# Optimization experiments

Hardware: AMD Instinct MI355X
Metric: run time of the kernel (lower is better)

## Reference

```python
import jax, jax.numpy as jnp
import numpy as np

B, L, DM = 4, 409, 192            # batch, tokens (1 cls + 16 target + 196 template + 196 search), d_model
DI, DS, DR, K, DEPTH = 384, 16, 12, 4, 24   # d_inner=2*DM, d_state, dt_rank=ceil(DM/16), d_conv, depth
EPS = 1e-5


def setup_inputs() -> dict:
    key = jax.random.key(0)
    ks = list(jax.random.split(key, 16))
    def rn(i, shape, s=0.02):
        return jax.random.normal(ks[i], shape, jnp.float32) * s
    # S4D-real init: A = [1..d_state] per channel, stored as log
    A_log = jnp.log(jnp.tile(jnp.arange(1, DS + 1, dtype=jnp.float32), (DEPTH, DI, 1)))
    return {
        "tokens": jax.random.normal(ks[0], (B, L, DM), jnp.float32),
        "norm_w": jnp.ones((DEPTH, DM), jnp.float32),
        "in_proj_w": rn(1, (DEPTH, 2 * DI, DM)),
        "conv_w": rn(2, (DEPTH, DI, 1, K), 0.2),
        "conv_b": jnp.zeros((DEPTH, DI), jnp.float32),
        "conv_w_b": rn(3, (DEPTH, DI, 1, K), 0.2),
        "conv_b_b": jnp.zeros((DEPTH, DI), jnp.float32),
        "x_proj_w": rn(4, (DEPTH, DR + 2 * DS, DI)),
        "x_proj_w_b": rn(5, (DEPTH, DR + 2 * DS, DI)),
        "dt_proj_w": rn(6, (DEPTH, DI, DR), 0.1),
        "dt_bias": rn(7, (DEPTH, DI), 0.5),
        "dt_proj_w_b": rn(8, (DEPTH, DI, DR), 0.1),
        "dt_bias_b": rn(9, (DEPTH, DI), 0.5),
        "A_log": A_log,
        "A_log_b": A_log,
        "D_param": jnp.ones((DEPTH, DI), jnp.float32),
        "D_param_b": jnp.ones((DEPTH, DI), jnp.float32),
        "out_proj_w": rn(10, (DEPTH, DM, DI)),
        "norm_f_w": jnp.ones((DM,), jnp.float32),
    }


def _rms(x, w):
    return x * jax.lax.rsqrt(jnp.mean(x * x, -1, keepdims=True) + EPS) * w


def _causal_conv(x, w, b):
    # x [B,L,DI]; depthwise causal conv1d, kernel K (pad left K-1)
    y = jax.lax.conv_general_dilated(
        jnp.swapaxes(x, 1, 2), w, (1,), [(K - 1, 0)],
        dimension_numbers=("NCH", "OIH", "NCH"), feature_group_count=DI)
    return jnp.swapaxes(y + b[None, :, None], 1, 2)


def _selective_scan(u, delta, A, Bm, Cm, Dp):
    # u,delta [B,L,DI]; A [DI,DS]; Bm,Cm [B,L,DS]; Dp [DI]
    def step(h, inp):
        u_t, d_t, b_t, c_t = inp  # [B,DI],[B,DI],[B,DS],[B,DS]
        h = h * jnp.exp(d_t[..., None] * A) + (d_t * u_t)[..., None] * b_t[:, None, :]
        return h, jnp.einsum("bdn,bn->bd", h, c_t)
    h0 = jnp.zeros((u.shape[0], A.shape[0], A.shape[1]), u.dtype)
    xs = tuple(jnp.swapaxes(t, 0, 1) for t in (u, delta, Bm, Cm))
    _, ys = jax.lax.scan(step, h0, xs)
    return jnp.swapaxes(ys, 0, 1) + u * Dp


def _scan_dir(xin, cw, cb, xpw, dtw, dtb, a_log, dp):
    xf = jax.nn.silu(_causal_conv(xin, cw, cb))
    x_dbl = jnp.einsum("bld,ed->ble", xf, xpw)
    dt, Bm, Cm = jnp.split(x_dbl, [DR, DR + DS], axis=-1)
    dt = jax.nn.softplus(jnp.einsum("blr,dr->bld", dt, dtw) + dtb)
    return _selective_scan(xf, dt, -jnp.exp(a_log), Bm, Cm, dp)


def _mixer(x, p):
    # bimamba v2: forward scan + backward (flipped) scan with separate params
    xz = jnp.einsum("bld,ed->ble", x, p["in_proj_w"])
    xin, z = jnp.split(xz, 2, axis=-1)
    y_f = _scan_dir(xin, p["conv_w"], p["conv_b"], p["x_proj_w"],
                    p["dt_proj_w"], p["dt_bias"], p["A_log"], p["D_param"])
    y_b = _scan_dir(xin[:, ::-1], p["conv_w_b"], p["conv_b_b"], p["x_proj_w_b"],
                    p["dt_proj_w_b"], p["dt_bias_b"], p["A_log_b"], p["D_param_b"])[:, ::-1]
    y = (y_f + y_b) * jax.nn.silu(z) * 0.5   # z-gating + if_divide_out
    return jnp.einsum("ble,de->bld", y, p["out_proj_w"])


def reference(tokens, norm_w, in_proj_w, conv_w, conv_b, conv_w_b, conv_b_b,
              x_proj_w, x_proj_w_b, dt_proj_w, dt_bias, dt_proj_w_b, dt_bias_b,
              A_log, A_log_b, D_param, D_param_b, out_proj_w, norm_f_w):
    stacked = {"norm_w": norm_w, "in_proj_w": in_proj_w,
               "conv_w": conv_w, "conv_b": conv_b, "conv_w_b": conv_w_b, "conv_b_b": conv_b_b,
               "x_proj_w": x_proj_w, "x_proj_w_b": x_proj_w_b,
               "dt_proj_w": dt_proj_w, "dt_bias": dt_bias,
               "dt_proj_w_b": dt_proj_w_b, "dt_bias_b": dt_bias_b,
               "A_log": A_log, "A_log_b": A_log_b,
               "D_param": D_param, "D_param_b": D_param_b,
               "out_proj_w": out_proj_w}

    def layer(carry, p):
        hidden, residual = carry
        residual = residual + hidden          # add (first layer: residual starts at 0)
        h = _rms(residual, p["norm_w"])       # fused_add_norm prenorm path (RMSNorm)
        h = _mixer(h, p)
        return (h, residual), None

    init = (tokens, jnp.zeros_like(tokens))
    (hidden, residual), _ = jax.lax.scan(layer, init, stacked)
    return _rms(residual + hidden, norm_f_w)
```

## Files before the change

### kernel.cpp

```cpp
#include <hip/hip_runtime.h>
#include <hip/hip_cooperative_groups.h>
#include <math.h>

namespace cg = cooperative_groups;

#define BB     4
#define LLEN   409
#define DMODEL 192
#define DINNER 384
#define DSTATE 16
#define DRANK  12
#define KCONV  4
#define NLAYER 24
#define NROW   (BB*LLEN)
#define EPSF   1e-5f
#define CH2    16
#define NCH2   26

#define OFF_A    12288
#define OFF_RS   16128
#define OFF_DTIN 16144
#define SMEMF    16336

#define NT_NORMIN  1236
#define NT_CONV    (2*NROW*96)
#define NT_XP2     206
#define NT_SCANP   312
#define NT_GATEOUT 309

__device__ __forceinline__ float siluf(float x){ return x/(1.f+__expf(-x)); }
__device__ __forceinline__ float softplusf(float x){ return (x>20.f)? x : log1pf(__expf(x)); }

struct MP {
  const float *norm_w, *conv_w, *conv_b, *conv_w_b, *conv_b_b;
  const float *dt_bias, *dt_bias_b, *D_param, *D_param_b, *norm_f_w;
  float *residual, *xz, *xf_f, *xf_b, *dtbc_f, *dtbc_b, *dt_f, *dt_b, *y_f, *y_b;
  float *q_buf, *sdt_buf;
  float *WtIn, *WtXpPF, *WtXpPB, *WtDtF, *WtDtB, *WtOut, *AnTF, *AnTB;
  float *out;
};

__global__ void k_init(const float* __restrict__ t, float* __restrict__ r, int n){
  int i = blockIdx.x*256+threadIdx.x;
  if (i<n) r[i]=t[i];
}

__global__ __launch_bounds__(256) void k_txp(const float* __restrict__ src,
    float* __restrict__ dst, int R, int C, int RP){
  __shared__ float t[32][33];
  int l = blockIdx.z;
  int c0 = blockIdx.x*32, r0 = blockIdx.y*32;
  const float* s = src + (size_t)l*R*C;
  float* d = dst + (size_t)l*C*RP;
  int tx = threadIdx.x, ty = threadIdx.y;
  #pragma unroll
  for (int yy=ty; yy<32; yy+=8){
    int rr = r0+yy, cc = c0+tx;
    t[yy][tx] = (rr<R && cc<C)? s[(size_t)rr*C+cc] : 0.f;
  }
  __syncthreads();
  #pragma unroll
  for (int yy=ty; yy<32; yy+=8){
    int cc = c0+yy, rr = r0+tx;
    if (cc<C && rr<RP) d[(size_t)cc*RP+rr] = t[tx][yy];
  }
}

__global__ void k_negexpT2(const float* __restrict__ a, float* __restrict__ o, int n){
  int i = blockIdx.x*256+threadIdx.x;
  if (i<n){
    int l = i/(DINNER*DSTATE); int rem = i%(DINNER*DSTATE);
    int nn = rem/DINNER, d = rem%DINNER;
    o[i] = -expf(a[((size_t)l*DINNER + d)*DSTATE + nn]);
  }
}

__device__ void ph_normin(float* sm, int task, int l, const MP& P){
  float* w_lds = sm;
  float* a_lds = sm + OFF_A;
  float* rs_s  = sm + OFF_RS;
  const float* norm_w = P.norm_w + (size_t)l*DMODEL;
  const float* Wt     = P.WtIn   + (size_t)l*DMODEL*768;
  int tid = threadIdx.x;
  int r0 = (task/12)*16, c0 = (task%12)*64;
  #pragma unroll
  for (int s=0;s<12;s++){
    int idx = tid + s*256; int i = idx/DMODEL, k = idx%DMODEL; int row = r0+i;
    a_lds[k*20+i] = (row<NROW)? P.residual[(size_t)row*DMODEL+k] : 0.f;
  }
  {
    int j4 = (tid&15)*4, kr = tid>>4;
    #pragma unroll
    for (int s=0;s<12;s++){
      int k = kr + s*16;
      *reinterpret_cast<float4*>(&w_lds[k*64+j4]) =
        *reinterpret_cast<const float4*>(&Wt[(size_t)k*768 + c0 + j4]);
    }
  }
  __syncthreads();
  int wv = tid>>6, lane = tid&63;
  {
    float ss[4] = {0.f,0.f,0.f,0.f};
    #pragma unroll
    for (int q=0;q<3;q++){
      int k = lane + q*64;
      #pragma unroll
      for (int r=0;r<4;r++){ float v = a_lds[k*20 + wv*4 + r]; ss[r] += v*v; }
    }
    #pragma unroll
    for (int r=0;r<4;r++){
      float s = ss[r];
      #pragma unroll
      for (int off=1; off<64; off<<=1) s += __shfl_xor(s, off, 64);
      if (lane==0) rs_s[wv*4+r] = rsqrtf(s/(float)DMODEL + EPSF);
    }
  }
  __syncthreads();
  #pragma unroll
  for (int s=0;s<12;s++){
    int idx = tid + s*256; int k = idx>>4, i = idx&15;
    a_lds[k*20+i] *= rs_s[i]*norm_w[k];
  }
  __syncthreads();
  int j = tid & 63, rg = tid >> 6;
  float acc[4] = {0.f,0.f,0.f,0.f};
  #pragma unroll 8
  for (int k=0;k<192;k++){
    float w = w_lds[k*64+j];
    float4 a = *reinterpret_cast<const float4*>(&a_lds[k*20 + rg*4]);
    acc[0]+=a.x*w; acc[1]+=a.y*w; acc[2]+=a.z*w; acc[3]+=a.w*w;
  }
  #pragma unroll
  for (int q=0;q<4;q++){
    int row = r0 + rg*4 + q;
    if (row<NROW) P.xz[(size_t)row*768 + c0 + j] = acc[q];
  }
  __syncthreads();
}

__device__ void ph_conv(int i, int l, const MP& P){
  int dir = i / (NROW*96);
  int rem = i - dir*(NROW*96);
  int d4 = (rem % 96)*4; int bl = rem / 96;
  int b = bl / LLEN; int ll = bl % LLEN;
  const float* cw = (dir? P.conv_w_b : P.conv_w) + (size_t)l*DINNER*KCONV;
  const float* cb = (dir? P.conv_b_b : P.conv_b) + (size_t)l*DINNER;
  float4 w0 = *reinterpret_cast<const float4*>(&cw[(d4+0)*KCONV]);
  float4 w1 = *reinterpret_cast<const float4*>(&cw[(d4+1)*KCONV]);
  float4 w2 = *reinterpret_cast<const float4*>(&cw[(d4+2)*KCONV]);
  float4 w3 = *reinterpret_cast<const float4*>(&cw[(d4+3)*KCONV]);
  float4 acc = *reinterpret_cast<const float4*>(&cb[d4]);
  const float* wa0 = (const float*)&w0; const float* wa1 = (const float*)&w1;
  const float* wa2 = (const float*)&w2; const float* wa3 = (const float*)&w3;
  #pragma unroll
  for (int k=0;k<KCONV;k++){
    int o = dir? (LLEN-1-ll-k+3) : (ll-3+k);
    bool ok = dir? (ll+k>=3) : (o>=0);
    if (ok){
      float4 x = *reinterpret_cast<const float4*>(&P.xz[((size_t)(b*LLEN+o))*768 + d4]);
      acc.x += wa0[k]*x.x; acc.y += wa1[k]*x.y; acc.z += wa2[k]*x.z; acc.w += wa3[k]*x.w;
    }
  }
  float* out = dir? P.xf_b : P.xf_f;
  float4 r; r.x = siluf(acc.x); r.y = siluf(acc.y); r.z = siluf(acc.z); r.w = siluf(acc.w);
  *reinterpret_cast<float4*>(&out[(size_t)bl*DINNER + d4]) = r;
}

__device__ void ph_xp2(float* sm, int task, int l, const MP& P){
  float* w_lds  = sm;
  float* a_lds  = sm + OFF_A;
  float* dtin_s = sm + OFF_DTIN;
  int dir = task & 1, rt = task >> 1;
  const float* xf  = dir? P.xf_b : P.xf_f;
  const float* Wxp = (dir? P.WtXpPB : P.WtXpPF) + (size_t)l*DINNER*64;
  const float* Wdt = (dir? P.WtDtB  : P.WtDtF ) + (size_t)l*DRANK*DINNER;
  const float* dtb = (dir? P.dt_bias_b : P.dt_bias) + (size_t)l*DINNER;
  float* dtbc = dir? P.dtbc_b : P.dtbc_f;
  float* dtp  = dir? P.dt_b   : P.dt_f;
  int tid = threadIdx.x, r0 = rt*16;
  int j = tid & 63, rg = tid >> 6;
  float acc[4] = {0.f,0.f,0.f,0.f};
  for (int c=0;c<2;c++){
    int K0 = c*192;
    if (c) __syncthreads();
    {
      int j4 = (tid&15)*4, kr = tid>>4;
      #pragma unroll
      for (int s=0;s<12;s++){
        int k = kr + s*16;
        *reinterpret_cast<float4*>(&w_lds[k*64+j4]) =
          *reinterpret_cast<const float4*>(&Wxp[(size_t)(K0+k)*64 + j4]);
      }
    }
    {
      int i = tid>>4, kc = (tid&15)*12;
      int row = r0+i;
      #pragma unroll
      for (int m=0;m<12;m+=4){
        float4 v = make_float4(0.f,0.f,0.f,0.f);
        if (row<NROW) v = *reinterpret_cast<const float4*>(&xf[(size_t)row*DINNER + K0 + kc + m]);
        a_lds[(kc+m+0)*20+i]=v.x; a_lds[(kc+m+1)*20+i]=v.y;
        a_lds[(kc+m+2)*20+i]=v.z; a_lds[(kc+m+3)*20+i]=v.w;
      }
    }
    __syncthreads();
    #pragma unroll 8
    for (int k=0;k<192;k++){
      float w = w_lds[k*64+j];
      float4 a = *reinterpret_cast<const float4*>(&a_lds[k*20 + rg*4]);
      acc[0]+=a.x*w; acc[1]+=a.y*w; acc[2]+=a.z*w; acc[3]+=a.w*w;
    }
  }
  __syncthreads();
  #pragma unroll
  for (int q=0;q<4;q++){
    int i = rg*4+q, row = r0+i;
    if (j<44 && row<NROW) dtbc[(size_t)row*44 + j] = acc[q];
    if (j<12) dtin_s[i*12 + j] = acc[q];
  }
  __syncthreads();
  for (int idx=tid; idx<12*DINNER; idx+=256) w_lds[idx] = Wdt[idx];
  __syncthreads();
  for (int idx=tid; idx<16*DINNER; idx+=256){
    int i = idx/DINNER, dd = idx - i*DINNER;
    int row = r0+i;
    float v = dtb[dd];
    #pragma unroll
    for (int r=0;r<12;r++) v += dtin_s[i*12+r]*w_lds[r*DINNER+dd];
    if (row<NROW) dtp[(size_t)row*DINNER+dd] = softplusf(v);
  }
  __syncthreads();
}

__device__ void ph_scan1(float* sm, int pair, int l, const MP& P){
  int tid = threadIdx.x;
  int sub = tid>>7, ltid = tid&127;
  int gt  = pair*2 + sub;
  int dir = gt / 312; int rem = gt % 312;
  int bch = rem / 3;  int d0b = rem % 3;
  int b = bch / NCH2, ch = bch % NCH2;
  const float* xf   = dir? P.xf_b  : P.xf_f;
  const float* dtbc = dir? P.dtbc_b: P.dtbc_f;
  const float* dtp  = dir? P.dt_b  : P.dt_f;
  const float* an   = (dir? P.AnTB : P.AnTF) + (size_t)l*DINNER*DSTATE;
  int t0 = ch*CH2;
  int T  = (t0+CH2<=LLEN)? CH2 : (LLEN-t0);
  int d0 = d0b*128;
  size_t base = (size_t)b*LLEN + t0;
  float* dt_s = sm + sub*5120;
  float* u_s  = dt_s + 2048;
  float* B_s  = dt_s + 4096;
  for (int t=0;t<T;t++){
    dt_s[t*128+ltid] = dtp[(base+t)*DINNER + d0 + ltid];
    u_s [t*128+ltid] = xf [(base+t)*DINNER + d0 + ltid];
  }
  for (int idx = ltid; idx < T*16; idx += 128){
    int t = idx>>4, n = idx&15;
    B_s[idx] = dtbc[(base+t)*44 + 12 + n];
  }
  __syncthreads();
  int d = d0 + ltid;
  float A[16], h[16];
  #pragma unroll
  for (int n=0;n<16;n++){ A[n] = an[n*DINNER + d]; h[n] = 0.f; }
  float sdt = 0.f;
  for (int t=0;t<T;t++){
    float dtv = dt_s[t*128+ltid];
    float du  = dtv * u_s[t*128+ltid];
    float Bv[16];
    #pragma unroll
    for (int q=0;q<4;q++) *reinterpret_cast<float4*>(&Bv[q*4]) =
        *reinterpret_cast<const float4*>(&B_s[t*16 + q*4]);
    #pragma unroll
    for (int n=0;n<16;n++) h[n] = h[n]*__expf(dtv*A[n]) + du*Bv[n];
    sdt += dtv;
  }
  size_t ci = ((size_t)dir*BB + b)*NCH2 + ch;
  float* qo = &P.q_buf[(ci*DINNER + d)*DSTATE];
  #pragma unroll
  for (int q=0;q<4;q++) *reinterpret_cast<float4*>(&qo[q*4]) =
      make_float4(h[q*4+0], h[q*4+1], h[q*4+2], h[q*4+3]);
  P.sdt_buf[ci*DINNER + d] = sdt;
  __syncthreads();
}

__device__ void ph_scan2(float* sm, int pair, int l, const MP& P){
  int tid = threadIdx.x;
  int sub = tid>>7, ltid = tid&127;
  int gt  = pair*2 + sub;
  int dir = gt / 312; int rem = gt % 312;
  int bch = rem / 3;  int d0b = rem % 3;
  int b = bch / NCH2, ch = bch % NCH2;
  const float* xf   = dir? P.xf_b  : P.xf_f;
  const float* dtbc = dir? P.dtbc_b: P.dtbc_f;
  const float* dtp  = dir? P.dt_b  : P.dt_f;
  const float* an   = (dir? P.AnTB : P.AnTF) + (size_t)l*DINNER*DSTATE;
  const float* Dp   = (dir? P.D_param_b : P.D_param) + (size_t)l*DINNER;
  float* y = dir? P.y_b : P.y_f;
  int t0 = ch*CH2;
  int T  = (t0+CH2<=LLEN)? CH2 : (LLEN-t0);
  int d0 = d0b*128;
  size_t base = (size_t)b*LLEN + t0;
  float* dt_s = sm + sub*5120;
  float* u_s  = dt_s + 2048;
  float* B_s  = dt_s + 4096;
  float* C_s  = dt_s + 4352;
  for (int t=0;t<T;t++){
    dt_s[t*128+ltid] = dtp[(base+t)*DINNER + d0 + ltid];
    u_s [t*128+ltid] = xf [(base+t)*DINNER + d0 + ltid];
  }
  for (int idx = ltid; idx < T*16; idx += 128){
    int t = idx>>4, n = idx&15;
    B_s[idx] = dtbc[(base+t)*44 + 12 + n];
    C_s[idx] = dtbc[(base+t)*44 + 28 + n];
  }
  __syncthreads();
  int d = d0 + ltid;
  float A[16], h[16];
  #pragma unroll
  for (int n=0;n<16;n++){ A[n] = an[n*DINNER + d]; h[n] = 0.f; }
  size_t sbase = ((size_t)dir*BB + b)*NCH2;
  for (int cc=0; cc<ch; cc++){
    float sv = P.sdt_buf[(sbase+cc)*DINNER + d];
    const float* qp = &P.q_buf[((sbase+cc)*DINNER + d)*DSTATE];
    #pragma unroll
    for (int n=0;n<16;n++) h[n] = qp[n] + __expf(A[n]*sv)*h[n];
  }
  float Dd = Dp[d];
  for (int t=0;t<T;t++){
    float dtv = dt_s[t*128+ltid];
    float u   = u_s [t*128+ltid];
    float du  = dtv*u;
    float Bv[16], Cv[16];
    #pragma unroll
    for (int q=0;q<4;q++){
      *reinterpret_cast<float4*>(&Bv[q*4]) = *reinterpret_cast<const float4*>(&B_s[t*16+q*4]);
      *reinterpret_cast<float4*>(&Cv[q*4]) = *reinterpret_cast<const float4*>(&C_s[t*16+q*4]);
    }
    float y0=0.f, y1=0.f, y2=0.f, y3=0.f;
    #pragma unroll
    for (int n=0;n<16;n+=4){
      h[n+0] = h[n+0]*__expf(dtv*A[n+0]) + du*Bv[n+0];
      h[n+1] = h[n+1]*__expf(dtv*A[n+1]) + du*Bv[n+1];
      h[n+2] = h[n+2]*__expf(dtv*A[n+2]) + du*Bv[n+2];
      h[n+3] = h[n+3]*__expf(dtv*A[n+3]) + du*Bv[n+3];
      y0 += h[n+0]*Cv[n+0]; y1 += h[n+1]*Cv[n+1];
      y2 += h[n+2]*Cv[n+2]; y3 += h[n+3]*Cv[n+3];
    }
    y[(base+t)*DINNER + d] = (y0+y1)+(y2+y3) + u*Dd;
  }
  __syncthreads();
}

__device__ void ph_gateout(float* sm, int task, int l, const MP& P){
  float* w_lds = sm;
  float* a_lds = sm + OFF_A;
  const float* Wt = P.WtOut + (size_t)l*DINNER*DMODEL;
  int tid = threadIdx.x;
  int r0 = (task/3)*16, c0 = (task%3)*64;
  int j = tid & 63, rg = tid >> 6;
  float acc[4] = {0.f,0.f,0.f,0.f};
  for (int c=0;c<2;c++){
    int K0 = c*192;
    if (c) __syncthreads();
    {
      int j4 = (tid&15)*4, kr = tid>>4;
      #pragma unroll
      for (int s=0;s<12;s++){
        int k = kr + s*16;
        *reinterpret_cast<float4*>(&w_lds[k*64+j4]) =
          *reinterpret_cast<const float4*>(&Wt[(size_t)(K0+k)*192 + c0 + j4]);
      }
    }
    #pragma unroll
    for (int s=0;s<12;s++){
      int idx = tid + s*256; int i = idx/192, k = idx - i*192;
      int row = r0+i; float v = 0.f;
      if (row<NROW){
        int b = row/LLEN, ll = row - b*LLEN;
        int rrow = b*LLEN + (LLEN-1-ll);
        float yf = P.y_f[(size_t)row*DINNER + K0 + k];
        float yb = P.y_b[(size_t)rrow*DINNER + K0 + k];
        float z  = P.xz[(size_t)row*768 + DINNER + K0 + k];
        v = (yf+yb)*siluf(z)*0.5f;
      }
      a_lds[k*20+i] = v;
    }
    __syncthreads();
    #pragma unroll 8
    for (int k=0;k<192;k++){
      float w = w_lds[k*64+j];
      float4 a = *reinterpret_cast<const float4*>(&a_lds[k*20 + rg*4]);
      acc[0]+=a.x*w; acc[1]+=a.y*w; acc[2]+=a.z*w; acc[3]+=a.w*w;
    }
  }
  #pragma unroll
  for (int q=0;q<4;q++){
    int row = r0 + rg*4 + q;
    if (row<NROW) P.residual[(size_t)row*DMODEL + c0 + j] += acc[q];
  }
  __syncthreads();
}

__device__ void ph_final(int row, const MP& P){
  int lane = threadIdx.x&63;
  float v[3]; float s = 0.f;
  #pragma unroll
  for (int q=0;q<3;q++){ v[q] = P.residual[(size_t)row*DMODEL + lane + q*64]; s += v[q]*v[q]; }
  #pragma unroll
  for (int off=1; off<64; off<<=1) s += __shfl_xor(s, off, 64);
  float sc = rsqrtf(s/(float)DMODEL + EPSF);
  #pragma unroll
  for (int q=0;q<3;q++) P.out[(size_t)row*DMODEL + lane + q*64] = v[q]*sc*P.norm_f_w[lane + q*64];
}

__global__ __launch_bounds__(256) void k_mega(MP P){
  cg::grid_group gg = cg::this_grid();
  __shared__ float sm[SMEMF];
  int nb = gridDim.x, bid = blockIdx.x, tid = threadIdx.x;
  for (int l=0; l<NLAYER; l++){
    for (int t=bid; t<NT_NORMIN; t+=nb) ph_normin(sm, t, l, P);
    gg.sync();
    for (int i=bid*256+tid; i<NT_CONV; i+=nb*256) ph_conv(i, l, P);
    gg.sync();
    for (int t=bid; t<NT_XP2; t+=nb) ph_xp2(sm, t, l, P);
    gg.sync();
    for (int t=bid; t<NT_SCANP; t+=nb) ph_scan1(sm, t, l, P);
    gg.sync();
    for (int t=bid; t<NT_SCANP; t+=nb) ph_scan2(sm, t, l, P);
    gg.sync();
    for (int t=bid; t<NT_GATEOUT; t+=nb) ph_gateout(sm, t, l, P);
    gg.sync();
  }
  for (int r = bid*4 + (tid>>6); r < NROW; r += nb*4) ph_final(r, P);
}

__global__ __launch_bounds__(256) void kw_normin(MP P, int l){
  __shared__ float sm[SMEMF];
  for (int t=blockIdx.x; t<NT_NORMIN; t+=gridDim.x) ph_normin(sm, t, l, P);
}
__global__ __launch_bounds__(256) void kw_conv(MP P, int l){
  for (int i=blockIdx.x*256+threadIdx.x; i<NT_CONV; i+=gridDim.x*256) ph_conv(i, l, P);
}
__global__ __launch_bounds__(256) void kw_xp2(MP P, int l){
  __shared__ float sm[SMEMF];
  for (int t=blockIdx.x; t<NT_XP2; t+=gridDim.x) ph_xp2(sm, t, l, P);
}
__global__ __launch_bounds__(256) void kw_scan1(MP P, int l){
  __shared__ float sm[SMEMF];
  for (int t=blockIdx.x; t<NT_SCANP; t+=gridDim.x) ph_scan1(sm, t, l, P);
}
__global__ __launch_bounds__(256) void kw_scan2(MP P, int l){
  __shared__ float sm[SMEMF];
  for (int t=blockIdx.x; t<NT_SCANP; t+=gridDim.x) ph_scan2(sm, t, l, P);
}
__global__ __launch_bounds__(256) void kw_gateout(MP P, int l){
  __shared__ float sm[SMEMF];
  for (int t=blockIdx.x; t<NT_GATEOUT; t+=gridDim.x) ph_gateout(sm, t, l, P);
}
__global__ __launch_bounds__(256) void kw_final(MP P){
  for (int r = blockIdx.x*4 + (threadIdx.x>>6); r < NROW; r += gridDim.x*4) ph_final(r, P);
}

extern "C" void kernel_launch(void* const* d_in, const int* in_sizes, int n_in,
                              void* d_out, int out_size, void* d_ws, size_t ws_size,
                              hipStream_t stream){
  const float* tokens     = (const float*)d_in[0];
  const float* norm_w     = (const float*)d_in[1];
  const float* in_proj_w  = (const float*)d_in[2];
  const float* conv_w     = (const float*)d_in[3];
  const float* conv_b     = (const float*)d_in[4];
  const float* conv_w_b   = (const float*)d_in[5];
  const float* conv_b_b   = (const float*)d_in[6];
  const float* x_proj_w   = (const float*)d_in[7];
  const float* x_proj_w_b = (const float*)d_in[8];
  const float* dt_proj_w  = (const float*)d_in[9];
  const float* dt_bias    = (const float*)d_in[10];
  const float* dt_proj_w_b= (const float*)d_in[11];
  const float* dt_bias_b  = (const float*)d_in[12];
  const float* A_log      = (const float*)d_in[13];
  const float* A_log_b    = (const float*)d_in[14];
  const float* D_param    = (const float*)d_in[15];
  const float* D_param_b  = (const float*)d_in[16];
  const float* out_proj_w = (const float*)d_in[17];
  const float* norm_f_w   = (const float*)d_in[18];

  float* ws = (float*)d_ws;
  size_t off = 0;
  float* residual = ws + off; off += (size_t)NROW*DMODEL;
  float* xz       = ws + off; off += (size_t)NROW*768;
  float* xf_f     = ws + off; off += (size_t)NROW*DINNER;
  float* xf_b     = ws + off; off += (size_t)NROW*DINNER;
  float* dtbc_f   = ws + off; off += (size_t)NROW*44;
  float* dtbc_b   = ws + off; off += (size_t)NROW*44;
  float* dt_f     = ws + off; off += (size_t)NROW*DINNER;
  float* dt_b     = ws + off; off += (size_t)NROW*DINNER;
  float* y_f      = ws + off; off += (size_t)NROW*DINNER;
  float* y_b      = ws + off; off += (size_t)NROW*DINNER;
  float* q_buf    = ws + off; off += (size_t)2*BB*NCH2*DINNER*DSTATE;
  float* sdt_buf  = ws + off; off += (size_t)2*BB*NCH2*DINNER;
  float* WtIn     = ws + off; off += (size_t)NLAYER*DMODEL*768;
  float* WtXpPF   = ws + off; off += (size_t)NLAYER*DINNER*64;
  float* WtXpPB   = ws + off; off += (size_t)NLAYER*DINNER*64;
  float* WtDtF    = ws + off; off += (size_t)NLAYER*DRANK*DINNER;
  float* WtDtB    = ws + off; off += (size_t)NLAYER*DRANK*DINNER;
  float* WtOut    = ws + off; off += (size_t)NLAYER*DINNER*DMODEL;
  float* AnTF     = ws + off; off += (size_t)NLAYER*DINNER*DSTATE;
  float* AnTB     = ws + off; off += (size_t)NLAYER*DINNER*DSTATE;
  if (off*sizeof(float) > ws_size) return;

  k_init<<<dim3((NROW*DMODEL+255)/256),256,0,stream>>>(tokens, residual, NROW*DMODEL);
  dim3 tb(32,8);
  k_txp<<<dim3(6,24,NLAYER),tb,0,stream>>>(in_proj_w,  WtIn,   768, 192, 768);
  k_txp<<<dim3(12,2,NLAYER),tb,0,stream>>>(x_proj_w,   WtXpPF,  44, 384,  64);
  k_txp<<<dim3(12,2,NLAYER),tb,0,stream>>>(x_proj_w_b, WtXpPB,  44, 384,  64);
  k_txp<<<dim3(1,12,NLAYER),tb,0,stream>>>(dt_proj_w,  WtDtF,  384,  12, 384);
  k_txp<<<dim3(1,12,NLAYER),tb,0,stream>>>(dt_proj_w_b,WtDtB,  384,  12, 384);
  k_txp<<<dim3(12,6,NLAYER),tb,0,stream>>>(out_proj_w, WtOut,  192, 384, 192);
  k_negexpT2<<<dim3((NLAYER*DINNER*DSTATE+255)/256),256,0,stream>>>(A_log,   AnTF, NLAYER*DINNER*DSTATE);
  k_negexpT2<<<dim3((NLAYER*DINNER*DSTATE+255)/256),256,0,stream>>>(A_log_b, AnTB, NLAYER*DINNER*DSTATE);

  MP P;
  P.norm_w = norm_w; P.conv_w = conv_w; P.conv_b = conv_b;
  P.conv_w_b = conv_w_b; P.conv_b_b = conv_b_b;
  P.dt_bias = dt_bias; P.dt_bias_b = dt_bias_b;
  P.D_param = D_param; P.D_param_b = D_param_b; P.norm_f_w = norm_f_w;
  P.residual = residual; P.xz = xz; P.xf_f = xf_f; P.xf_b = xf_b;
  P.dtbc_f = dtbc_f; P.dtbc_b = dtbc_b; P.dt_f = dt_f; P.dt_b = dt_b;
  P.y_f = y_f; P.y_b = y_b; P.q_buf = q_buf; P.sdt_buf = sdt_buf;
  P.WtIn = WtIn; P.WtXpPF = WtXpPF; P.WtXpPB = WtXpPB;
  P.WtDtF = WtDtF; P.WtDtB = WtDtB; P.WtOut = WtOut;
  P.AnTF = AnTF; P.AnTB = AnTB;
  P.out = (float*)d_out;

  int coopOK = 0;
  int dev = 0; hipGetDevice(&dev);
  hipDeviceProp_t prop;
  if (hipGetDeviceProperties(&prop, dev) == hipSuccess && prop.cooperativeLaunch){
    int maxb = 0;
    if (hipOccupancyMaxActiveBlocksPerMultiprocessor(&maxb, k_mega, 256, 0) == hipSuccess && maxb > 0){
      int nblk = maxb * prop.multiProcessorCount;
      if (nblk > 512) nblk = 512;
      if (nblk >= 64){
        void* args[] = { (void*)&P };
        hipError_t e = hipLaunchCooperativeKernel((const void*)k_mega,
            dim3(nblk), dim3(256), args, 0, stream);
        if (e == hipSuccess) coopOK = 1;
      }
    }
  }
  if (!coopOK){
    for (int l=0; l<NLAYER; l++){
      kw_normin <<<dim3(NT_NORMIN),256,0,stream>>>(P, l);
      kw_conv   <<<dim3((NT_CONV+255)/256),256,0,stream>>>(P, l);
      kw_xp2    <<<dim3(NT_XP2),256,0,stream>>>(P, l);
      kw_scan1  <<<dim3(NT_SCANP),256,0,stream>>>(P, l);
      kw_scan2  <<<dim3(NT_SCANP),256,0,stream>>>(P, l);
      kw_gateout<<<dim3(NT_GATEOUT),256,0,stream>>>(P, l);
    }
    kw_final<<<dim3((NROW+3)/4),256,0,stream>>>(P);
  }
}
```

Baseline: 2.844 ms.

## Fuse causal conv into x_proj phase, shrink shared memory, raise occupancy

Folds the depthwise causal conv plus SiLU into the x_proj/dt phase, so each block computes its 16 rows of conv output directly into shared memory. This removes one grid-wide sync and a separate pass per layer. The GEMM tiles become row-major activations with K-chunks of 48 weights, which cuts shared memory from about 64KB to 40KB. Launch bounds now request 3 blocks per CU and the cooperative grid cap rises to 1024 blocks. The trade-offs are more grid-sync participants, more K-chunk barriers, and reading the dt_proj weights straight from global memory instead of staging them.

```diff
diff --git a/kernel.cpp b/kernel.cpp
--- a/kernel.cpp
+++ b/kernel.cpp
@@ -17,14 +17,10 @@
 #define CH2    16
 #define NCH2   26
 
-#define OFF_A    12288
-#define OFF_RS   16128
-#define OFF_DTIN 16144
-#define SMEMF    16336
+#define SMEMF 10240
 
 #define NT_NORMIN  1236
-#define NT_CONV    (2*NROW*96)
-#define NT_XP2     206
+#define NT_XPC     206
 #define NT_SCANP   312
 #define NT_GATEOUT 309
 
@@ -76,59 +72,64 @@
 }
 
 __device__ void ph_normin(float* sm, int task, int l, const MP& P){
-  float* w_lds = sm;
-  float* a_lds = sm + OFF_A;
-  float* rs_s  = sm + OFF_RS;
-  const float* norm_w = P.norm_w + (size_t)l*DMODEL;
-  const float* Wt     = P.WtIn   + (size_t)l*DMODEL*768;
+  float* a_s = sm;
+  float* w_s = sm + 3200;
+  float* rs_s = sm + 6272;
+  const float* nw = P.norm_w + (size_t)l*DMODEL;
+  const float* Wt = P.WtIn   + (size_t)l*DMODEL*768;
   int tid = threadIdx.x;
   int r0 = (task/12)*16, c0 = (task%12)*64;
   #pragma unroll
-  for (int s=0;s<12;s++){
-    int idx = tid + s*256; int i = idx/DMODEL, k = idx%DMODEL; int row = r0+i;
-    a_lds[k*20+i] = (row<NROW)? P.residual[(size_t)row*DMODEL+k] : 0.f;
-  }
-  {
-    int j4 = (tid&15)*4, kr = tid>>4;
-    #pragma unroll
-    for (int s=0;s<12;s++){
-      int k = kr + s*16;
-      *reinterpret_cast<float4*>(&w_lds[k*64+j4]) =
-        *reinterpret_cast<const float4*>(&Wt[(size_t)k*768 + c0 + j4]);
-    }
+  for (int u=0; u<3; u++){
+    int idx = tid + u*256;
+    int i = idx/48, k4 = (idx%48)*4;
+    int row = r0+i;
+    float4 v = make_float4(0.f,0.f,0.f,0.f);
+    if (row<NROW) v = *(const float4*)&P.residual[(size_t)row*DMODEL + k4];
+    *(float4*)&a_s[i*200+k4] = v;
   }
   __syncthreads();
   int wv = tid>>6, lane = tid&63;
-  {
-    float ss[4] = {0.f,0.f,0.f,0.f};
-    #pragma unroll
-    for (int q=0;q<3;q++){
-      int k = lane + q*64;
-      #pragma unroll
-      for (int r=0;r<4;r++){ float v = a_lds[k*20 + wv*4 + r]; ss[r] += v*v; }
-    }
-    #pragma unroll
-    for (int r=0;r<4;r++){
-      float s = ss[r];
-      #pragma unroll
-      for (int off=1; off<64; off<<=1) s += __shfl_xor(s, off, 64);
-      if (lane==0) rs_s[wv*4+r] = rsqrtf(s/(float)DMODEL + EPSF);
-    }
-  }
-  __syncthreads();
-  #pragma unroll
-  for (int s=0;s<12;s++){
-    int idx = tid + s*256; int k = idx>>4, i = idx&15;
-    a_lds[k*20+i] *= rs_s[i]*norm_w[k];
-  }
-  __syncthreads();
-  int j = tid & 63, rg = tid >> 6;
+  #pragma unroll
+  for (int r=0;r<4;r++){
+    int i = wv*4+r;
+    float s = 0.f;
+    #pragma unroll
+    for (int q=0;q<3;q++){ float v = a_s[i*200 + lane + q*64]; s += v*v; }
+    #pragma unroll
+    for (int o=1;o<64;o<<=1) s += __shfl_xor(s,o,64);
+    if (lane==0) rs_s[i] = rsqrtf(s/(float)DMODEL + EPSF);
+  }
+  __syncthreads();
+  #pragma unroll
+  for (int u=0;u<12;u++){
+    int idx = tid + u*256; int i = idx/192, k = idx%192;
+    a_s[i*200+k] *= rs_s[i]*nw[k];
+  }
+  __syncthreads();
+  int j = tid&63, rg = tid>>6;
   float acc[4] = {0.f,0.f,0.f,0.f};
-  #pragma unroll 8
-  for (int k=0;k<192;k++){
-    float w = w_lds[k*64+j];
-    float4 a = *reinterpret_cast<const float4*>(&a_lds[k*20 + rg*4]);
-    acc[0]+=a.x*w; acc[1]+=a.y*w; acc[2]+=a.z*w; acc[3]+=a.w*w;
+  for (int c=0;c<4;c++){
+    int K0 = c*48;
+    {
+      int j4 = (tid&15)*4, kr = tid>>4;
+      #pragma unroll
+      for (int s2=0;s2<3;s2++){
+        int kk = kr + s2*16;
+        *(float4*)&w_s[kk*64+j4] = *(const float4*)&Wt[(size_t)(K0+kk)*768 + c0 + j4];
+      }
+    }
+    __syncthreads();
+    #pragma unroll 4
+    for (int kk=0;kk<48;kk+=4){
+      float w0=w_s[kk*64+j], w1=w_s[(kk+1)*64+j], w2=w_s[(kk+2)*64+j], w3=w_s[(kk+3)*64+j];
+      #pragma unroll
+      for (int q=0;q<4;q++){
+        float4 av = *(const float4*)&a_s[(rg*4+q)*200 + K0 + kk];
+        acc[q] += av.x*w0 + av.y*w1 + av.z*w2 + av.w*w3;
+      }
+    }
+    __syncthreads();
   }
   #pragma unroll
   for (int q=0;q<4;q++){
@@ -138,80 +139,75 @@
   __syncthreads();
 }
 
-__device__ void ph_conv(int i, int l, const MP& P){
-  int dir = i / (NROW*96);
-  int rem = i - dir*(NROW*96);
-  int d4 = (rem % 96)*4; int bl = rem / 96;
-  int b = bl / LLEN; int ll = bl % LLEN;
-  const float* cw = (dir? P.conv_w_b : P.conv_w) + (size_t)l*DINNER*KCONV;
-  const float* cb = (dir? P.conv_b_b : P.conv_b) + (size_t)l*DINNER;
-  float4 w0 = *reinterpret_cast<const float4*>(&cw[(d4+0)*KCONV]);
-  float4 w1 = *reinterpret_cast<const float4*>(&cw[(d4+1)*KCONV]);
-  float4 w2 = *reinterpret_cast<const float4*>(&cw[(d4+2)*KCONV]);
-  float4 w3 = *reinterpret_cast<const float4*>(&cw[(d4+3)*KCONV]);
-  float4 acc = *reinterpret_cast<const float4*>(&cb[d4]);
-  const float* wa0 = (const float*)&w0; const float* wa1 = (const float*)&w1;
-  const float* wa2 = (const float*)&w2; const float* wa3 = (const float*)&w3;
-  #pragma unroll
-  for (int k=0;k<KCONV;k++){
-    int o = dir? (LLEN-1-ll-k+3) : (ll-3+k);
-    bool ok = dir? (ll+k>=3) : (o>=0);
-    if (ok){
-      float4 x = *reinterpret_cast<const float4*>(&P.xz[((size_t)(b*LLEN+o))*768 + d4]);
-      acc.x += wa0[k]*x.x; acc.y += wa1[k]*x.y; acc.z += wa2[k]*x.z; acc.w += wa3[k]*x.w;
-    }
-  }
-  float* out = dir? P.xf_b : P.xf_f;
-  float4 r; r.x = siluf(acc.x); r.y = siluf(acc.y); r.z = siluf(acc.z); r.w = siluf(acc.w);
-  *reinterpret_cast<float4*>(&out[(size_t)bl*DINNER + d4]) = r;
-}
-
-__device__ void ph_xp2(float* sm, int task, int l, const MP& P){
-  float* w_lds  = sm;
-  float* a_lds  = sm + OFF_A;
-  float* dtin_s = sm + OFF_DTIN;
+__device__ void ph_xp2conv(float* sm, int task, int l, const MP& P){
+  float* a_s    = sm;
+  float* w_s    = sm + 6272;
+  float* dtin_s = sm + 9344;
   int dir = task & 1, rt = task >> 1;
-  const float* xf  = dir? P.xf_b : P.xf_f;
+  const float* cw  = (dir? P.conv_w_b : P.conv_w) + (size_t)l*DINNER*KCONV;
+  const float* cb  = (dir? P.conv_b_b : P.conv_b) + (size_t)l*DINNER;
   const float* Wxp = (dir? P.WtXpPB : P.WtXpPF) + (size_t)l*DINNER*64;
   const float* Wdt = (dir? P.WtDtB  : P.WtDtF ) + (size_t)l*DRANK*DINNER;
   const float* dtb = (dir? P.dt_bias_b : P.dt_bias) + (size_t)l*DINNER;
-  float* dtbc = dir? P.dtbc_b : P.dtbc_f;
-  float* dtp  = dir? P.dt_b   : P.dt_f;
+  float* xf   = dir? P.xf_b  : P.xf_f;
+  float* dtbc = dir? P.dtbc_b: P.dtbc_f;
+  float* dtp  = dir? P.dt_b  : P.dt_f;
   int tid = threadIdx.x, r0 = rt*16;
-  int j = tid & 63, rg = tid >> 6;
+  #pragma unroll
+  for (int u=0;u<6;u++){
+    int idx = tid + u*256;
+    int i = idx/96, d4 = (idx%96)*4;
+    int row = r0+i;
+    float4 v = make_float4(0.f,0.f,0.f,0.f);
+    if (row<NROW){
+      int b = row/LLEN, ll = row - b*LLEN;
+      float4 w0 = *(const float4*)&cw[(d4+0)*KCONV];
+      float4 w1 = *(const float4*)&cw[(d4+1)*KCONV];
+      float4 w2 = *(const float4*)&cw[(d4+2)*KCONV];
+      float4 w3 = *(const float4*)&cw[(d4+3)*KCONV];
+      float4 acc = *(const float4*)&cb[d4];
+      const float* pa0=(const float*)&w0; const float* pa1=(const float*)&w1;
+      const float* pa2=(const float*)&w2; const float* pa3=(const float*)&w3;
+      #pragma unroll
+      for (int k=0;k<KCONV;k++){
+        int o = dir? (LLEN-1-ll-k+3) : (ll-3+k);
+        bool ok = dir? (ll+k>=3) : (o>=0);
+        if (ok){
+          float4 x = *(const float4*)&P.xz[((size_t)(b*LLEN+o))*768 + d4];
+          acc.x += pa0[k]*x.x; acc.y += pa1[k]*x.y;
+          acc.z += pa2[k]*x.z; acc.w += pa3[k]*x.w;
+        }
+      }
+      v.x = siluf(acc.x); v.y = siluf(acc.y); v.z = siluf(acc.z); v.w = siluf(acc.w);
+      *(float4*)&xf[(size_t)row*DINNER + d4] = v;
+    }
+    *(float4*)&a_s[i*392+d4] = v;
+  }
+  __syncthreads();
+  int j = tid&63, rg = tid>>6;
   float acc[4] = {0.f,0.f,0.f,0.f};
-  for (int c=0;c<2;c++){
-    int K0 = c*192;
-    if (c) __syncthreads();
+  for (int c=0;c<8;c++){
+    int K0 = c*48;
     {
       int j4 = (tid&15)*4, kr = tid>>4;
       #pragma unroll
-      for (int s=0;s<12;s++){
-        int k = kr + s*16;
-        *reinterpret_cast<float4*>(&w_lds[k*64+j4]) =
-          *reinterpret_cast<const float4*>(&Wxp[(size_t)(K0+k)*64 + j4]);
-      }
-    }
-    {
-      int i = tid>>4, kc = (tid&15)*12;
-      int row = r0+i;
-      #pragma unroll
-      for (int m=0;m<12;m+=4){
-        float4 v = make_float4(0.f,0.f,0.f,0.f);
-        if (row<NROW) v = *reinterpret_cast<const float4*>(&xf[(size_t)row*DINNER + K0 + kc + m]);
-        a_lds[(kc+m+0)*20+i]=v.x; a_lds[(kc+m+1)*20+i]=v.y;
-        a_lds[(kc+m+2)*20+i]=v.z; a_lds[(kc+m+3)*20+i]=v.w;
+      for (int s2=0;s2<3;s2++){
+        int kk = kr + s2*16;
+        *(float4*)&w_s[kk*64+j4] = *(const float4*)&Wxp[(size_t)(K0+kk)*64 + j4];
       }
     }
     __syncthreads();
-    #pragma unroll 8
-    for (int k=0;k<192;k++){
-      float w = w_lds[k*64+j];
-      float4 a = *reinterpret_cast<const float4*>(&a_lds[k*20 + rg*4]);
-      acc[0]+=a.x*w; acc[1]+=a.y*w; acc[2]+=a.z*w; acc[3]+=a.w*w;
-    }
-  }
-  __syncthreads();
+    #pragma unroll 4
+    for (int kk=0;kk<48;kk+=4){
+      float w0=w_s[kk*64+j], w1=w_s[(kk+1)*64+j], w2=w_s[(kk+2)*64+j], w3=w_s[(kk+3)*64+j];
+      #pragma unroll
+      for (int q=0;q<4;q++){
+        float4 av = *(const float4*)&a_s[(rg*4+q)*392 + K0 + kk];
+        acc[q] += av.x*w0 + av.y*w1 + av.z*w2 + av.w*w3;
+      }
+    }
+    __syncthreads();
+  }
   #pragma unroll
   for (int q=0;q<4;q++){
     int i = rg*4+q, row = r0+i;
@@ -219,15 +215,17 @@
     if (j<12) dtin_s[i*12 + j] = acc[q];
   }
   __syncthreads();
-  for (int idx=tid; idx<12*DINNER; idx+=256) w_lds[idx] = Wdt[idx];
-  __syncthreads();
-  for (int idx=tid; idx<16*DINNER; idx+=256){
-    int i = idx/DINNER, dd = idx - i*DINNER;
+  #pragma unroll
+  for (int u=0;u<24;u++){
+    int idx = tid + u*256;
+    int i = idx/384, dd = idx - i*384;
     int row = r0+i;
-    float v = dtb[dd];
-    #pragma unroll
-    for (int r=0;r<12;r++) v += dtin_s[i*12+r]*w_lds[r*DINNER+dd];
-    if (row<NROW) dtp[(size_t)row*DINNER+dd] = softplusf(v);
+    if (row<NROW){
+      float v = dtb[dd];
+      #pragma unroll
+      for (int r=0;r<12;r++) v += dtin_s[i*12+r]*Wdt[(size_t)r*DINNER+dd];
+      dtp[(size_t)row*DINNER+dd] = softplusf(v);
+    }
   }
   __syncthreads();
 }
@@ -353,46 +351,52 @@
 }
 
 __device__ void ph_gateout(float* sm, int task, int l, const MP& P){
-  float* w_lds = sm;
-  float* a_lds = sm + OFF_A;
+  float* a_s = sm;
+  float* w_s = sm + 6272;
   const float* Wt = P.WtOut + (size_t)l*DINNER*DMODEL;
   int tid = threadIdx.x;
   int r0 = (task/3)*16, c0 = (task%3)*64;
-  int j = tid & 63, rg = tid >> 6;
+  #pragma unroll
+  for (int u=0;u<6;u++){
+    int idx = tid + u*256;
+    int i = idx/96, d4 = (idx%96)*4;
+    int row = r0+i;
+    float4 v = make_float4(0.f,0.f,0.f,0.f);
+    if (row<NROW){
+      int b = row/LLEN, ll = row - b*LLEN;
+      int rrow = b*LLEN + (LLEN-1-ll);
+      float4 yf = *(const float4*)&P.y_f[(size_t)row*DINNER + d4];
+      float4 yb = *(const float4*)&P.y_b[(size_t)rrow*DINNER + d4];
+      float4 z  = *(const float4*)&P.xz[(size_t)row*768 + DINNER + d4];
+      v.x = (yf.x+yb.x)*siluf(z.x)*0.5f; v.y = (yf.y+yb.y)*siluf(z.y)*0.5f;
+      v.z = (yf.z+yb.z)*siluf(z.z)*0.5f; v.w = (yf.w+yb.w)*siluf(z.w)*0.5f;
+    }
+    *(float4*)&a_s[i*392+d4] = v;
+  }
+  __syncthreads();
+  int j = tid&63, rg = tid>>6;
   float acc[4] = {0.f,0.f,0.f,0.f};
-  for (int c=0;c<2;c++){
-    int K0 = c*192;
-    if (c) __syncthreads();
+  for (int c=0;c<8;c++){
+    int K0 = c*48;
     {
       int j4 = (tid&15)*4, kr = tid>>4;
       #pragma unroll
-      for (int s=0;s<12;s++){
-        int k = kr + s*16;
-        *reinterpret_cast<float4*>(&w_lds[k*64+j4]) =
-          *reinterpret_cast<const float4*>(&Wt[(size_t)(K0+k)*192 + c0 + j4]);
-      }
-    }
-    #pragma unroll
-    for (int s=0;s<12;s++){
-      int idx = tid + s*256; int i = idx/192, k = idx - i*192;
-      int row = r0+i; float v = 0.f;
-      if (row<NROW){
-        int b = row/LLEN, ll = row - b*LLEN;
-        int rrow = b*LLEN + (LLEN-1-ll);
-        float yf = P.y_f[(size_t)row*DINNER + K0 + k];
-        float yb = P.y_b[(size_t)rrow*DINNER + K0 + k];
-        float z  = P.xz[(size_t)row*768 + DINNER + K0 + k];
-        v = (yf+yb)*siluf(z)*0.5f;
-      }
-      a_lds[k*20+i] = v;
+      for (int s2=0;s2<3;s2++){
+        int kk = kr + s2*16;
+        *(float4*)&w_s[kk*64+j4] = *(const float4*)&Wt[(size_t)(K0+kk)*192 + c0 + j4];
+      }
     }
     __syncthreads();
-    #pragma unroll 8
-    for (int k=0;k<192;k++){
-      float w = w_lds[k*64+j];
-      float4 a = *reinterpret_cast<const float4*>(&a_lds[k*20 + rg*4]);
-      acc[0]+=a.x*w; acc[1]+=a.y*w; acc[2]+=a.z*w; acc[3]+=a.w*w;
-    }
+    #pragma unroll 4
+    for (int kk=0;kk<48;kk+=4){
+      float w0=w_s[kk*64+j], w1=w_s[(kk+1)*64+j], w2=w_s[(kk+2)*64+j], w3=w_s[(kk+3)*64+j];
+      #pragma unroll
+      for (int q=0;q<4;q++){
+        float4 av = *(const float4*)&a_s[(rg*4+q)*392 + K0 + kk];
+        acc[q] += av.x*w0 + av.y*w1 + av.z*w2 + av.w*w3;
+      }
+    }
+    __syncthreads();
   }
   #pragma unroll
   for (int q=0;q<4;q++){
@@ -408,22 +412,20 @@
   #pragma unroll
   for (int q=0;q<3;q++){ v[q] = P.residual[(size_t)row*DMODEL + lane + q*64]; s += v[q]*v[q]; }
   #pragma unroll
-  for (int off=1; off<64; off<<=1) s += __shfl_xor(s, off, 64);
+  for (int o=1;o<64;o<<=1) s += __shfl_xor(s,o,64);
   float sc = rsqrtf(s/(float)DMODEL + EPSF);
   #pragma unroll
   for (int q=0;q<3;q++) P.out[(size_t)row*DMODEL + lane + q*64] = v[q]*sc*P.norm_f_w[lane + q*64];
 }
 
-__global__ __launch_bounds__(256) void k_mega(MP P){
+__global__ __launch_bounds__(256,3) void k_mega(MP P){
   cg::grid_group gg = cg::this_grid();
   __shared__ float sm[SMEMF];
   int nb = gridDim.x, bid = blockIdx.x, tid = threadIdx.x;
   for (int l=0; l<NLAYER; l++){
     for (int t=bid; t<NT_NORMIN; t+=nb) ph_normin(sm, t, l, P);
     gg.sync();
-    for (int i=bid*256+tid; i<NT_CONV; i+=nb*256) ph_conv(i, l, P);
-    gg.sync();
-    for (int t=bid; t<NT_XP2; t+=nb) ph_xp2(sm, t, l, P);
+    for (int t=bid; t<NT_XPC; t+=nb) ph_xp2conv(sm, t, l, P);
     gg.sync();
     for (int t=bid; t<NT_SCANP; t+=nb) ph_scan1(sm, t, l, P);
     gg.sync();
@@ -435,26 +437,23 @@
   for (int r = bid*4 + (tid>>6); r < NROW; r += nb*4) ph_final(r, P);
 }
 
-__global__ __launch_bounds__(256) void kw_normin(MP P, int l){
+__global__ __launch_bounds__(256,3) void kw_normin(MP P, int l){
   __shared__ float sm[SMEMF];
   for (int t=blockIdx.x; t<NT_NORMIN; t+=gridDim.x) ph_normin(sm, t, l, P);
 }
-__global__ __launch_bounds__(256) void kw_conv(MP P, int l){
-  for (int i=blockIdx.x*256+threadIdx.x; i<NT_CONV; i+=gridDim.x*256) ph_conv(i, l, P);
-}
-__global__ __launch_bounds__(256) void kw_xp2(MP P, int l){
+__global__ __launch_bounds__(256,3) void kw_xp2conv(MP P, int l){
   __shared__ float sm[SMEMF];
-  for (int t=blockIdx.x; t<NT_XP2; t+=gridDim.x) ph_xp2(sm, t, l, P);
-}
-__global__ __launch_bounds__(256) void kw_scan1(MP P, int l){
+  for (int t=blockIdx.x; t<NT_XPC; t+=gridDim.x) ph_xp2conv(sm, t, l, P);
+}
+__global__ __launch_bounds__(256,3) void kw_scan1(MP P, int l){
   __shared__ float sm[SMEMF];
   for (int t=blockIdx.x; t<NT_SCANP; t+=gridDim.x) ph_scan1(sm, t, l, P);
 }
-__global__ __launch_bounds__(256) void kw_scan2(MP P, int l){
+__global__ __launch_bounds__(256,3) void kw_scan2(MP P, int l){
   __shared__ float sm[SMEMF];
   for (int t=blockIdx.x; t<NT_SCANP; t+=gridDim.x) ph_scan2(sm, t, l, P);
 }
-__global__ __launch_bounds__(256) void kw_gateout(MP P, int l){
+__global__ __launch_bounds__(256,3) void kw_gateout(MP P, int l){
   __shared__ float sm[SMEMF];
   for (int t=blockIdx.x; t<NT_GATEOUT; t+=gridDim.x) ph_gateout(sm, t, l, P);
 }
@@ -540,7 +539,7 @@
     int maxb = 0;
     if (hipOccupancyMaxActiveBlocksPerMultiprocessor(&maxb, k_mega, 256, 0) == hipSuccess && maxb > 0){
       int nblk = maxb * prop.multiProcessorCount;
-      if (nblk > 512) nblk = 512;
+      if (nblk > 1024) nblk = 1024;
       if (nblk >= 64){
         void* args[] = { (void*)&P };
         hipError_t e = hipLaunchCooperativeKernel((const void*)k_mega,
@@ -552,8 +551,7 @@
   if (!coopOK){
     for (int l=0; l<NLAYER; l++){
       kw_normin <<<dim3(NT_NORMIN),256,0,stream>>>(P, l);
-      kw_conv   <<<dim3((NT_CONV+255)/256),256,0,stream>>>(P, l);
-      kw_xp2    <<<dim3(NT_XP2),256,0,stream>>>(P, l);
+      kw_xp2conv<<<dim3(NT_XPC),256,0,stream>>>(P, l);
       kw_scan1  <<<dim3(NT_SCANP),256,0,stream>>>(P, l);
       kw_scan2  <<<dim3(NT_SCANP),256,0,stream>>>(P, l);
       kw_gateout<<<dim3(NT_GATEOUT),256,0,stream>>>(P, l);
```

Result: slower. 9.333 ms (+228.2%).
